# Performance work log

Measured on AMD Instinct MI355X. Metric: run time of the kernel, lower is better.

Reference implementation:

```python
import jax, jax.numpy as jnp
import numpy as np

N_NODES = 100000
N_EDGES = 1600000
IN_F = 128
HEADS1, HID = 8, 8
N_CLASSES = 40


def setup_inputs() -> dict:
    key = jax.random.key(0)
    ks = jax.random.split(key, 12)
    x = jax.random.normal(ks[0], (N_NODES, IN_F), dtype=jnp.float32)
    edge_index = jax.random.randint(ks[1], (2, N_EDGES), 0, N_NODES, dtype=jnp.int32)
    edge_attr = jax.random.uniform(ks[2], (N_EDGES, 1), dtype=jnp.float32)
    s = 0.1
    W1 = jax.random.normal(ks[3], (IN_F, HEADS1 * HID), dtype=jnp.float32) * s
    att_src1 = jax.random.normal(ks[4], (HEADS1, HID), dtype=jnp.float32) * s
    att_dst1 = jax.random.normal(ks[5], (HEADS1, HID), dtype=jnp.float32) * s
    att_edge1 = jax.random.normal(ks[6], (1, HEADS1), dtype=jnp.float32) * s
    W2 = jax.random.normal(ks[7], (HEADS1 * HID, N_CLASSES), dtype=jnp.float32) * s
    att_src2 = jax.random.normal(ks[8], (1, N_CLASSES), dtype=jnp.float32) * s
    att_dst2 = jax.random.normal(ks[9], (1, N_CLASSES), dtype=jnp.float32) * s
    att_edge2 = jax.random.normal(ks[10], (1, 1), dtype=jnp.float32) * s
    return {"x": x, "edge_index": edge_index, "edge_attr": edge_attr,
            "W1": W1, "att_src1": att_src1, "att_dst1": att_dst1, "att_edge1": att_edge1,
            "W2": W2, "att_src2": att_src2, "att_dst2": att_dst2, "att_edge2": att_edge2}


def _egat(x, src, dst, edge_attr, W, a_src, a_dst, a_edge, heads, out_dim, concat):
    """Edge-featured GAT conv: gather -> per-edge attention -> neighborhood softmax -> scatter."""
    n = x.shape[0]
    h = (x @ W).reshape(n, heads, out_dim)                       # [N,H,F]
    h_src = h[src]                                               # [E,H,F]
    logits = (h_src * a_src).sum(-1) + (h[dst] * a_dst).sum(-1)  # [E,H]
    logits = logits + edge_attr @ a_edge                          # edge feature term
    logits = jax.nn.leaky_relu(logits, 0.2)
    m = jax.ops.segment_max(logits, dst, num_segments=n)         # [N,H]
    e = jnp.exp(logits - m[dst])
    denom = jax.ops.segment_sum(e, dst, num_segments=n)
    alpha = e / (denom[dst] + 1e-16)                             # softmax over incoming edges
    out = jax.ops.segment_sum(alpha[:, :, None] * h_src, dst, num_segments=n)  # [N,H,F]
    return out.reshape(n, heads * out_dim) if concat else out.mean(axis=1)


def reference(x, edge_index, edge_attr, W1, att_src1, att_dst1, att_edge1,
              W2, att_src2, att_dst2, att_edge2):
    src, dst = edge_index[0], edge_index[1]
    h = _egat(x, src, dst, edge_attr, W1, att_src1, att_dst1, att_edge1, HEADS1, HID, True)
    h = jax.nn.elu(h)
    out = _egat(h, src, dst, edge_attr, W2, att_src2, att_dst2, att_edge2, 1, N_CLASSES, True)
    return jax.nn.log_softmax(out, axis=1)
```

## Files before the change

### kernel.cpp

```cpp
#include <hip/hip_runtime.h>
#include <math.h>

#define N_NODES 100000
#define N_EDGES 1600000
#define IN_F    128
#define NH1     8
#define HID     8
#define C1      64
#define C2      40

#define EB      2048
#define B1      ((N_EDGES + EB - 1) / EB)
#define NPB     128
#define NBIN    ((N_NODES + NPB - 1) / NPB)
#define S2CAP   2560

#define WPREP_BLKS 44
#define GEMM1_BLKS ((N_NODES / 16 + 3) / 4)

typedef unsigned short ushort_t;
typedef unsigned int uint_t;
typedef _Float16 half_t;
typedef short short8 __attribute__((ext_vector_type(8)));
typedef float f32x4 __attribute__((ext_vector_type(4)));

__device__ __forceinline__ float lrelu(float x) { return x > 0.f ? x : 0.2f * x; }
__device__ __forceinline__ ushort_t f2bf(float f) {
    uint_t u = __float_as_uint(f);
    u = (u + 0x7FFFu + ((u >> 16) & 1u)) >> 16;
    return (ushort_t)u;
}
__device__ __forceinline__ float bf2f(ushort_t s) {
    return __uint_as_float(((uint_t)s) << 16);
}
__device__ __forceinline__ short8 ld8f2bf(const float* p) {
    float4 a = *(const float4*)p;
    float4 b = *(const float4*)(p + 4);
    ushort_t o[8] = {f2bf(a.x), f2bf(a.y), f2bf(a.z), f2bf(a.w),
                     f2bf(b.x), f2bf(b.y), f2bf(b.z), f2bf(b.w)};
    return *(const short8*)o;
}

__global__ __launch_bounds__(256) void k_prep_hist(
    const float* __restrict__ W1, ushort_t* __restrict__ W1p,
    const float* __restrict__ W2, ushort_t* __restrict__ W2p,
    const int* __restrict__ ei, int* __restrict__ Hblk)
{
    int b = blockIdx.x;
    if (b < B1) {
        __shared__ int h[NBIN];
        for (int i = threadIdx.x; i < NBIN; i += 256) h[i] = 0;
        __syncthreads();
        int base = b * EB;
        for (int i = threadIdx.x; i < EB; i += 256) {
            int idx = base + i;
            if (idx < N_EDGES) atomicAdd(&h[((uint_t)ei[N_EDGES + idx]) >> 7], 1);
        }
        __syncthreads();
        for (int i = threadIdx.x; i < NBIN; i += 256)
            Hblk[i * B1 + b] = h[i];
        return;
    }
    int i = (b - B1) * 256 + threadIdx.x;
    if (i < 8192) {
        int j = i & 7, lane = (i >> 3) & 63, nt = (i >> 9) & 3, s = i >> 11;
        int k = s * 32 + (lane >> 4) * 8 + j;
        int n = nt * 16 + (lane & 15);
        W1p[i] = f2bf(W1[k * C1 + n]);
    } else {
        int i2 = i - 8192;
        if (i2 < 3072) {
            int j = i2 & 7, lane = (i2 >> 3) & 63, khalf = (i2 >> 9) & 1, nt = i2 >> 10;
            int n = nt * 16 + (lane & 15);
            int k = khalf * 32 + (lane >> 4) * 8 + j;
            float v = (n < C2) ? W2[k * C2 + n] : 0.f;
            W2p[i2] = f2bf(v);
        }
    }
}

__global__ __launch_bounds__(512) void k_colscan(
    int* __restrict__ Hblk, int* __restrict__ totB)
{
    __shared__ int s[512];
    int bin = blockIdx.x, t = threadIdx.x;
    int run = 0;
    for (int c = 0; c < 2; ++c) {
        int i = c * 512 + t;
        int v = (i < B1) ? Hblk[bin * B1 + i] : 0;
        s[t] = v;
        __syncthreads();
        for (int off = 1; off < 512; off <<= 1) {
            int u = (t >= off) ? s[t - off] : 0;
            __syncthreads();
            s[t] += u;
            __syncthreads();
        }
        if (i < B1) Hblk[bin * B1 + i] = s[t] - v + run;
        int tot = s[511];
        __syncthreads();
        run += tot;
    }
    if (t == 0) totB[bin] = run;
}

__global__ __launch_bounds__(512) void k_basescan(
    const int* __restrict__ totB, int* __restrict__ baseB,
    int* __restrict__ rowptr)
{
    __shared__ int s[512];
    int t = threadIdx.x;
    int run = 0;
    for (int c = 0; c < 2; ++c) {
        int i = c * 512 + t;
        int v = (i < NBIN) ? totB[i] : 0;
        s[t] = v;
        __syncthreads();
        for (int off = 1; off < 512; off <<= 1) {
            int u = (t >= off) ? s[t - off] : 0;
            __syncthreads();
            s[t] += u;
            __syncthreads();
        }
        if (i < NBIN) baseB[i] = s[t] - v + run;
        int tot = s[511];
        __syncthreads();
        run += tot;
    }
    if (t == 0) { baseB[NBIN] = run; rowptr[N_NODES] = run; }
}

__global__ __launch_bounds__(256) void k_gemm1_sc1(
    const float* __restrict__ x, const ushort_t* __restrict__ W1p,
    const float* __restrict__ as1, const float* __restrict__ ad1,
    ushort_t* __restrict__ H1, float* __restrict__ s1, float* __restrict__ d1,
    const int* __restrict__ ei, const float* __restrict__ ea,
    const int* __restrict__ Hblk, const int* __restrict__ baseB,
    int2* __restrict__ coarse)
{
    int b = blockIdx.x;
    int t = threadIdx.x;
    if (b < B1) {
        __shared__ int    cnt[NBIN];
        __shared__ int    loff[NBIN];
        __shared__ int    gof[NBIN];
        __shared__ int    ssc[256];
        __shared__ int2   sbuf[EB];
        __shared__ ushort_t sbin[EB];
        int base = b * EB;
        int nE = min(EB, N_EDGES - base);
        for (int i = t; i < NBIN; i += 256) cnt[i] = 0;
        __syncthreads();
        int myb[EB / 256];
        #pragma unroll
        for (int c = 0; c < EB / 256; ++c) {
            int i = base + c * 256 + t;
            int bn = -1;
            if (i < N_EDGES) {
                bn = ((uint_t)ei[N_EDGES + i]) >> 7;
                atomicAdd(&cnt[bn], 1);
            }
            myb[c] = bn;
        }
        __syncthreads();
        {
            int b4 = t * 4;
            int a0 = (b4 + 0 < NBIN) ? cnt[b4 + 0] : 0;
            int a1 = (b4 + 1 < NBIN) ? cnt[b4 + 1] : 0;
            int a2 = (b4 + 2 < NBIN) ? cnt[b4 + 2] : 0;
            int a3 = (b4 + 3 < NBIN) ? cnt[b4 + 3] : 0;
            int tsum = a0 + a1 + a2 + a3;
            ssc[t] = tsum;
            __syncthreads();
            for (int off = 1; off < 256; off <<= 1) {
                int u = (t >= off) ? ssc[t - off] : 0;
                __syncthreads();
                ssc[t] += u;
                __syncthreads();
            }
            int exc = ssc[t] - tsum;
            if (b4 + 0 < NBIN) loff[b4 + 0] = exc;
            if (b4 + 1 < NBIN) loff[b4 + 1] = exc + a0;
            if (b4 + 2 < NBIN) loff[b4 + 2] = exc + a0 + a1;
            if (b4 + 3 < NBIN) loff[b4 + 3] = exc + a0 + a1 + a2;
        }
        __syncthreads();
        for (int i = t; i < NBIN; i += 256) {
            gof[i] = baseB[i] + Hblk[i * B1 + b] - loff[i];
            cnt[i] = loff[i];
        }
        __syncthreads();
        #pragma unroll
        for (int c = 0; c < EB / 256; ++c) {
            int i = base + c * 256 + t;
            if (i < N_EDGES) {
                int bn = myb[c];
                int s = ei[i];
                int d = ei[N_EDGES + i];
                float e = ea[i];
                int p = atomicAdd(&cnt[bn], 1);
                sbuf[p] = make_int2(s | ((d & (NPB - 1)) << 24), __float_as_int(e));
                sbin[p] = (ushort_t)bn;
            }
        }
        __syncthreads();
        for (int j = t; j < nE; j += 256) {
            int bn = sbin[j];
            coarse[gof[bn] + j] = sbuf[j];
        }
        return;
    }
    int tile = ((b - B1) * 256 + t) >> 6;
    int lane = t & 63;
    if (tile >= N_NODES / 16) return;
    int quad = lane >> 4, lo = lane & 15;
    const float* arow = x + ((size_t)tile * 16 + lo) * IN_F + quad * 8;
    short8 a0 = ld8f2bf(arow);
    short8 a1 = ld8f2bf(arow + 32);
    short8 a2 = ld8f2bf(arow + 64);
    short8 a3 = ld8f2bf(arow + 96);
    f32x4 acc[4] = {{0,0,0,0},{0,0,0,0},{0,0,0,0},{0,0,0,0}};
    #pragma unroll
    for (int nt = 0; nt < 4; ++nt) {
        short8 b0 = *(const short8*)&W1p[((0 * 4 + nt) * 64 + lane) * 8];
        short8 b1 = *(const short8*)&W1p[((1 * 4 + nt) * 64 + lane) * 8];
        short8 b2 = *(const short8*)&W1p[((2 * 4 + nt) * 64 + lane) * 8];
        short8 b3 = *(const short8*)&W1p[((3 * 4 + nt) * 64 + lane) * 8];
        acc[nt] = __builtin_amdgcn_mfma_f32_16x16x32_bf16(a0, b0, acc[nt], 0, 0, 0);
        acc[nt] = __builtin_amdgcn_mfma_f32_16x16x32_bf16(a1, b1, acc[nt], 0, 0, 0);
        acc[nt] = __builtin_amdgcn_mfma_f32_16x16x32_bf16(a2, b2, acc[nt], 0, 0, 0);
        acc[nt] = __builtin_amdgcn_mfma_f32_16x16x32_bf16(a3, b3, acc[nt], 0, 0, 0);
    }
    int nb = tile * 16 + quad * 4;
    float ps[4][4], pd[4][4];
    #pragma unroll
    for (int nt = 0; nt < 4; ++nt) {
        int cb = nt * 16 + lo;
        float av = as1[cb], dv = ad1[cb];
        #pragma unroll
        for (int r = 0; r < 4; ++r) {
            H1[(size_t)(nb + r) * C1 + cb] = f2bf(acc[nt][r]);
            ps[nt][r] = acc[nt][r] * av;
            pd[nt][r] = acc[nt][r] * dv;
        }
    }
    #pragma unroll
    for (int nt = 0; nt < 4; ++nt)
        #pragma unroll
        for (int r = 0; r < 4; ++r)
            #pragma unroll
            for (int off = 1; off < 8; off <<= 1) {
                ps[nt][r] += __shfl_xor(ps[nt][r], off);
                pd[nt][r] += __shfl_xor(pd[nt][r], off);
            }
    if ((lo & 7) == 0) {
        int hh = lo >> 3;
        #pragma unroll
        for (int nt = 0; nt < 4; ++nt) {
            int h = nt * 2 + hh;
            #pragma unroll
            for (int r = 0; r < 4; ++r) {
                s1[(nb + r) * NH1 + h] = ps[nt][r];
                d1[(nb + r) * NH1 + h] = pd[nt][r];
            }
        }
    }
}

__global__ __launch_bounds__(256) void k_scatter2(
    const int2* __restrict__ coarse, const int* __restrict__ baseB,
    int2* __restrict__ edges, int* __restrict__ rowptr)
{
    __shared__ int2 buf[S2CAP];
    __shared__ int h[NPB];
    __shared__ int ofx[NPB];
    __shared__ int ssc[256];
    int bin = blockIdx.x, t = threadIdx.x;
    int s0 = baseB[bin], s1b = baseB[bin + 1];
    int n = s1b - s0;
    if (t < NPB) h[t] = 0;
    __syncthreads();
    for (int j = t; j < n; j += 256)
        atomicAdd(&h[(uint_t)coarse[s0 + j].x >> 24], 1);
    __syncthreads();
    int v = (t < NPB) ? h[t] : 0;
    ssc[t] = v;
    __syncthreads();
    for (int off = 1; off < 256; off <<= 1) {
        int u = (t >= off) ? ssc[t - off] : 0;
        __syncthreads();
        ssc[t] += u;
        __syncthreads();
    }
    int exc = ssc[t] - v;
    if (t < NPB) {
        ofx[t] = exc;
        int node = bin * NPB + t;
        if (node < N_NODES) rowptr[node] = s0 + exc;
        h[t] = exc;
    }
    __syncthreads();
    for (int j = t; j < n; j += 256) {
        int2 c = coarse[s0 + j];
        int ln = (uint_t)c.x >> 24;
        int p = atomicAdd(&h[ln], 1);
        int2 ov = make_int2(c.x & 0x00FFFFFF, c.y);
        if (p < S2CAP) buf[p] = ov;
        else           edges[s0 + p] = ov;
    }
    __syncthreads();
    int nl = n < S2CAP ? n : S2CAP;
    for (int j = t; j < nl; j += 256)
        edges[s0 + j] = buf[j];
}


__global__ __launch_bounds__(256) void k_node1(
    const int* __restrict__ rowptr, const int2* __restrict__ edges,
    const float* __restrict__ s1, const float* __restrict__ d1,
    const float* __restrict__ ae1,
    const ushort_t* __restrict__ H1, ushort_t* __restrict__ out1r)
{
    __shared__ uint_t sm_s[4][64];
    __shared__ float  sm_pf[4][8][65];
    int w = (blockIdx.x * blockDim.x + threadIdx.x) >> 6;
    int lane = threadIdx.x & 63;
    int wv = (threadIdx.x >> 6) & 3;
    if (w >= N_NODES) return;
    int half = lane >> 5, lo32 = lane & 31;
    int h = lo32 >> 2;
    uint_t fb = (uint_t)lo32 << 2;
    int jb = rowptr[w], je = rowptr[w + 1];
    float4 d1a = *(const float4*)(d1 + w * NH1);
    float4 d1b = *(const float4*)(d1 + w * NH1 + 4);
    float4 aea = *(const float4*)(ae1);
    float4 aeb = *(const float4*)(ae1 + 4);
    float den = 0.f, acc0 = 0.f, acc1 = 0.f;
    const float* pfh = sm_pf[wv][h];
    for (int base = jb; base < je; base += 64) {
        int idx = base + lane;
        uint_t soff = 0;
        float pf[8] = {0.f, 0.f, 0.f, 0.f, 0.f, 0.f, 0.f, 0.f};
        if (idx < je) {
            int2 ed = edges[idx];
            soff = (uint_t)ed.x << 7;
            float ea = __int_as_float(ed.y);
            const float* s1r = s1 + (size_t)ed.x * NH1;
            float4 sa = *(const float4*)s1r;
            float4 sb = *(const float4*)(s1r + 4);
            pf[0] = __expf(lrelu(fmaf(ea, aea.x, sa.x + d1a.x)));
            pf[1] = __expf(lrelu(fmaf(ea, aea.y, sa.y + d1a.y)));
            pf[2] = __expf(lrelu(fmaf(ea, aea.z, sa.z + d1a.z)));
            pf[3] = __expf(lrelu(fmaf(ea, aea.w, sa.w + d1a.w)));
            pf[4] = __expf(lrelu(fmaf(ea, aeb.x, sb.x + d1b.x)));
            pf[5] = __expf(lrelu(fmaf(ea, aeb.y, sb.y + d1b.y)));
            pf[6] = __expf(lrelu(fmaf(ea, aeb.z, sb.z + d1b.z)));
            pf[7] = __expf(lrelu(fmaf(ea, aeb.w, sb.w + d1b.w)));
        }
        sm_s[wv][lane] = soff;
        #pragma unroll
        for (int k = 0; k < 8; ++k) sm_pf[wv][k][lane] = pf[k];
        __builtin_amdgcn_wave_barrier();
        int cnt4 = (min(64, je - base) + 3) & ~3;
        for (int e = half; e < cnt4; e += 4) {
            uint_t soA = sm_s[wv][e];
            uint_t soB = sm_s[wv][e + 2];
            float pA = pfh[e];
            float pB = pfh[e + 2];
            uint_t uA = *(const uint_t*)((const char*)H1 + (soA + fb));
            uint_t uB = *(const uint_t*)((const char*)H1 + (soB + fb));
            den += pA + pB;
            acc0 = fmaf(pA, __uint_as_float(uA << 16), acc0);
            acc1 = fmaf(pA, __uint_as_float(uA & 0xffff0000u), acc1);
            acc0 = fmaf(pB, __uint_as_float(uB << 16), acc0);
            acc1 = fmaf(pB, __uint_as_float(uB & 0xffff0000u), acc1);
        }
        __builtin_amdgcn_wave_barrier();
    }
    acc0 += __shfl_xor(acc0, 32);
    acc1 += __shfl_xor(acc1, 32);
    den  += __shfl_xor(den, 32);
    float inv = 1.f / (den + 1e-16f);
    float o0 = acc0 * inv, o1 = acc1 * inv;
    float r0 = o0 > 0.f ? o0 : __expf(o0) - 1.f;
    float r1 = o1 > 0.f ? o1 : __expf(o1) - 1.f;
    if (half == 0) {
        uint_t pk = (uint_t)f2bf(r0) | ((uint_t)f2bf(r1) << 16);
        *(uint_t*)((char*)out1r + (size_t)w * 128 + fb) = pk;
    }
}

__global__ __launch_bounds__(256) void k_gemm2(
    const ushort_t* __restrict__ out1r, const ushort_t* __restrict__ W2p,
    const float* __restrict__ as2, const float* __restrict__ ad2,
    ushort_t* __restrict__ H2, float* __restrict__ s2, float* __restrict__ d2)
{
    int tile = (blockIdx.x * blockDim.x + threadIdx.x) >> 6;
    int lane = threadIdx.x & 63;
    if (tile >= N_NODES / 16) return;
    int quad = lane >> 4, lo = lane & 15;
    const ushort_t* arow = out1r + ((size_t)tile * 16 + lo) * C1 + quad * 8;
    short8 a0 = *(const short8*)arow;
    short8 a1 = *(const short8*)(arow + 32);
    f32x4 acc[3] = {{0,0,0,0},{0,0,0,0},{0,0,0,0}};
    #pragma unroll
    for (int nt = 0; nt < 3; ++nt) {
        short8 b0 = *(const short8*)&W2p[((nt * 2 + 0) * 64 + lane) * 8];
        short8 b1 = *(const short8*)&W2p[((nt * 2 + 1) * 64 + lane) * 8];
        acc[nt] = __builtin_amdgcn_mfma_f32_16x16x32_bf16(a0, b0, acc[nt], 0, 0, 0);
        acc[nt] = __builtin_amdgcn_mfma_f32_16x16x32_bf16(a1, b1, acc[nt], 0, 0, 0);
    }
    float ps0 = 0.f, ps1 = 0.f, ps2 = 0.f, ps3 = 0.f;
    float pd0 = 0.f, pd1 = 0.f, pd2 = 0.f, pd3 = 0.f;
    #pragma unroll
    for (int nt = 0; nt < 3; ++nt) {
        int cb = nt * 16 + lo;
        float a2 = cb < C2 ? as2[cb] : 0.f;
        float b2 = cb < C2 ? ad2[cb] : 0.f;
        float v0 = acc[nt][0], v1 = acc[nt][1], v2 = acc[nt][2], v3 = acc[nt][3];
        int nb = tile * 16 + quad * 4;
        H2[(size_t)(nb + 0) * C1 + cb] = f2bf(v0);
        H2[(size_t)(nb + 1) * C1 + cb] = f2bf(v1);
        H2[(size_t)(nb + 2) * C1 + cb] = f2bf(v2);
        H2[(size_t)(nb + 3) * C1 + cb] = f2bf(v3);
        ps0 = fmaf(v0, a2, ps0); ps1 = fmaf(v1, a2, ps1);
        ps2 = fmaf(v2, a2, ps2); ps3 = fmaf(v3, a2, ps3);
        pd0 = fmaf(v0, b2, pd0); pd1 = fmaf(v1, b2, pd1);
        pd2 = fmaf(v2, b2, pd2); pd3 = fmaf(v3, b2, pd3);
    }
    #pragma unroll
    for (int off = 1; off < 16; off <<= 1) {
        ps0 += __shfl_xor(ps0, off); ps1 += __shfl_xor(ps1, off);
        ps2 += __shfl_xor(ps2, off); ps3 += __shfl_xor(ps3, off);
        pd0 += __shfl_xor(pd0, off); pd1 += __shfl_xor(pd1, off);
        pd2 += __shfl_xor(pd2, off); pd3 += __shfl_xor(pd3, off);
    }
    if (lo == 0) {
        int nb = tile * 16 + quad * 4;
        s2[nb + 0] = ps0; s2[nb + 1] = ps1; s2[nb + 2] = ps2; s2[nb + 3] = ps3;
        d2[nb + 0] = pd0; d2[nb + 1] = pd1; d2[nb + 2] = pd2; d2[nb + 3] = pd3;
    }
}

__global__ __launch_bounds__(256) void k_node2(
    const int* __restrict__ rowptr, const int2* __restrict__ edges,
    const float* __restrict__ s2, const float* __restrict__ d2,
    const float* __restrict__ ae2,
    const ushort_t* __restrict__ H2, float* __restrict__ out)
{
    __shared__ int2 sp[4][64];
    int w = (blockIdx.x * blockDim.x + threadIdx.x) >> 6;
    int lane = threadIdx.x & 63;
    int wv = (threadIdx.x >> 6) & 3;
    if (w >= N_NODES) return;
    int half = lane >> 5, lo32 = lane & 31;
    int fi = lo32 < 20 ? lo32 : 19;
    uint_t fb = (uint_t)fi << 2;
    int jb = rowptr[w], je = rowptr[w + 1];
    float d2v = d2[w];
    float aev = ae2[0];
    float den = 0.f, acc0 = 0.f, acc1 = 0.f;
    for (int base = jb; base < je; base += 64) {
        int idx = base + lane;
        int soff = 0; float p = 0.f;
        if (idx < je) {
            int2 ed = edges[idx];
            soff = ed.x << 7;
            p = __expf(lrelu(s2[ed.x] + d2v + __int_as_float(ed.y) * aev));
        }
        sp[wv][lane] = make_int2(soff, __float_as_int(p));
        __builtin_amdgcn_wave_barrier();
        int cnt4 = (min(64, je - base) + 3) & ~3;
        for (int e = half; e < cnt4; e += 4) {
            int2 edA = sp[wv][e];
            int2 edB = sp[wv][e + 2];
            uint_t uA = *(const uint_t*)((const char*)H2 + ((uint_t)edA.x + fb));
            uint_t uB = *(const uint_t*)((const char*)H2 + ((uint_t)edB.x + fb));
            float pA = __int_as_float(edA.y);
            float pB = __int_as_float(edB.y);
            den += pA + pB;
            acc0 = fmaf(pA, __uint_as_float(uA << 16), acc0);
            acc1 = fmaf(pA, __uint_as_float(uA & 0xffff0000u), acc1);
            acc0 = fmaf(pB, __uint_as_float(uB << 16), acc0);
            acc1 = fmaf(pB, __uint_as_float(uB & 0xffff0000u), acc1);
        }
        __builtin_amdgcn_wave_barrier();
    }
    acc0 += __shfl_xor(acc0, 32);
    acc1 += __shfl_xor(acc1, 32);
    den  += __shfl_xor(den, 32);
    float inv = 1.f / (den + 1e-16f);
    float o0 = acc0 * inv, o1 = acc1 * inv;
    float v0 = lo32 < 20 ? o0 : -INFINITY;
    float v1 = lo32 < 20 ? o1 : -INFINITY;
    float m = fmaxf(v0, v1);
    #pragma unroll
    for (int off = 16; off; off >>= 1) m = fmaxf(m, __shfl_xor(m, off));
    float pp = lo32 < 20 ? __expf(v0 - m) + __expf(v1 - m) : 0.f;
    #pragma unroll
    for (int off = 16; off; off >>= 1) pp += __shfl_xor(pp, off);
    float ls = __logf(pp);
    if (half == 0 && lo32 < 20) {
        float2 st = make_float2(v0 - m - ls, v1 - m - ls);
        *(float2*)(out + (size_t)w * C2 + 2 * fi) = st;
    }
}

extern "C" void kernel_launch(void* const* d_in, const int* in_sizes, int n_in,
                              void* d_out, int out_size, void* d_ws, size_t ws_size,
                              hipStream_t stream)
{
    const float* x   = (const float*)d_in[0];
    const int*   ei  = (const int*)  d_in[1];
    const float* ea  = (const float*)d_in[2];
    const float* W1  = (const float*)d_in[3];
    const float* as1 = (const float*)d_in[4];
    const float* ad1 = (const float*)d_in[5];
    const float* ae1 = (const float*)d_in[6];
    const float* W2  = (const float*)d_in[7];
    const float* as2 = (const float*)d_in[8];
    const float* ad2 = (const float*)d_in[9];
    const float* ae2 = (const float*)d_in[10];
    float* out = (float*)d_out;

    float*    ws     = (float*)d_ws;
    ushort_t* H1     = (ushort_t*)ws;
    ushort_t* H2     = (ushort_t*)ws;
    ushort_t* out1r  = (ushort_t*)(ws + 3200000);
    int*      Hblk   = (int*)(ws + 3200000);
    int*      totB   = (int*)(ws + 3820000);
    int*      baseB  = (int*)(ws + 3821000);
    int2*     coarse = (int2*)(ws + 6400000);
    int2*     edges  = (int2*)(ws + 9600000);
    float*    s1     = ws + 16000000;
    float*    d1     = ws + 16800000;
    int*      rowptr = (int*)(ws + 17600000);
    float*    s2     = ws + 17700008;
    float*    d2     = ws + 17800008;
    ushort_t* W2p    = (ushort_t*)(ws + 17900008);
    ushort_t* W1p    = (ushort_t*)(ws + 17901544);

    k_prep_hist <<<B1 + WPREP_BLKS, 256, 0, stream>>>(
        W1, W1p, W2, W2p, ei, Hblk);
    k_colscan   <<<NBIN, 512, 0, stream>>>(Hblk, totB);
    k_basescan  <<<1, 512, 0, stream>>>(totB, baseB, rowptr);
    k_gemm1_sc1 <<<B1 + GEMM1_BLKS, 256, 0, stream>>>(
        x, W1p, as1, ad1, H1, s1, d1, ei, ea, Hblk, baseB, coarse);
    k_scatter2  <<<NBIN, 256, 0, stream>>>(coarse, baseB, edges, rowptr);
    k_node1     <<<(N_NODES + 3) / 4, 256, 0, stream>>>(rowptr, edges, s1, d1, ae1,
                                                        H1, out1r);
    k_gemm2     <<<(N_NODES / 16 + 3) / 4, 256, 0, stream>>>(out1r, W2p, as2, ad2,
                                                             H2, s2, d2);
    k_node2     <<<(N_NODES + 3) / 4, 256, 0, stream>>>(rowptr, edges, s2, d2, ae2,
                                                        H2, out);
}
```

Before: 286.3 us.

## Process two nodes per wavefront in GAT aggregation kernels and transpose histogram layout

The per-node aggregation kernels now map two destination nodes onto one 64-lane wavefront, each half-wave handling one node's edges in chunks of 32. The cross-half shuffle reduction goes away and the grid is halved. With an average degree of 16, this should waste fewer lanes than one node per wave with 64-edge chunks. The per-block histogram matrix is also transposed to block-major, so the histogram writes and the scatter reads become contiguous while the column scan reads become strided. The risk is divergence when the two paired nodes have very different degrees, since both halves loop to the larger count.

```diff
diff --git a/kernel.cpp b/kernel.cpp
--- a/kernel.cpp
+++ b/kernel.cpp
@@ -17,6 +17,7 @@
 
 #define WPREP_BLKS 44
 #define GEMM1_BLKS ((N_NODES / 16 + 3) / 4)
+#define NPAIR   (N_NODES / 2)
 
 typedef unsigned short ushort_t;
 typedef unsigned int uint_t;
@@ -58,7 +59,7 @@
         }
         __syncthreads();
         for (int i = threadIdx.x; i < NBIN; i += 256)
-            Hblk[i * B1 + b] = h[i];
+            Hblk[b * NBIN + i] = h[i];
         return;
     }
     int i = (b - B1) * 256 + threadIdx.x;
@@ -87,7 +88,7 @@
     int run = 0;
     for (int c = 0; c < 2; ++c) {
         int i = c * 512 + t;
-        int v = (i < B1) ? Hblk[bin * B1 + i] : 0;
+        int v = (i < B1) ? Hblk[i * NBIN + bin] : 0;
         s[t] = v;
         __syncthreads();
         for (int off = 1; off < 512; off <<= 1) {
@@ -96,7 +97,7 @@
             s[t] += u;
             __syncthreads();
         }
-        if (i < B1) Hblk[bin * B1 + i] = s[t] - v + run;
+        if (i < B1) Hblk[i * NBIN + bin] = s[t] - v + run;
         int tot = s[511];
         __syncthreads();
         run += tot;
@@ -186,7 +187,7 @@
         }
         __syncthreads();
         for (int i = t; i < NBIN; i += 256) {
-            gof[i] = baseB[i] + Hblk[i * B1 + b] - loff[i];
+            gof[i] = baseB[i] + Hblk[b * NBIN + i] - loff[i];
             cnt[i] = loff[i];
         }
         __syncthreads();
@@ -273,7 +274,6 @@
 {
     __shared__ int2 buf[S2CAP];
     __shared__ int h[NPB];
-    __shared__ int ofx[NPB];
     __shared__ int ssc[256];
     int bin = blockIdx.x, t = threadIdx.x;
     int s0 = baseB[bin], s1b = baseB[bin + 1];
@@ -294,7 +294,6 @@
     }
     int exc = ssc[t] - v;
     if (t < NPB) {
-        ofx[t] = exc;
         int node = bin * NPB + t;
         if (node < N_NODES) rowptr[node] = s0 + exc;
         h[t] = exc;
@@ -321,28 +320,31 @@
     const float* __restrict__ ae1,
     const ushort_t* __restrict__ H1, ushort_t* __restrict__ out1r)
 {
-    __shared__ uint_t sm_s[4][64];
-    __shared__ float  sm_pf[4][8][65];
-    int w = (blockIdx.x * blockDim.x + threadIdx.x) >> 6;
+    __shared__ uint_t sm_s[4][2][33];
+    __shared__ float  sm_pf[4][2][8][33];
+    int w2 = (blockIdx.x * blockDim.x + threadIdx.x) >> 6;
     int lane = threadIdx.x & 63;
     int wv = (threadIdx.x >> 6) & 3;
-    if (w >= N_NODES) return;
+    if (w2 >= NPAIR) return;
     int half = lane >> 5, lo32 = lane & 31;
+    int node = 2 * w2 + half;
     int h = lo32 >> 2;
     uint_t fb = (uint_t)lo32 << 2;
-    int jb = rowptr[w], je = rowptr[w + 1];
-    float4 d1a = *(const float4*)(d1 + w * NH1);
-    float4 d1b = *(const float4*)(d1 + w * NH1 + 4);
+    int jb = rowptr[node], je = rowptr[node + 1];
+    int cnt = je - jb;
+    int maxc = max(cnt, __shfl_xor(cnt, 32));
+    float4 d1a = *(const float4*)(d1 + node * NH1);
+    float4 d1b = *(const float4*)(d1 + node * NH1 + 4);
     float4 aea = *(const float4*)(ae1);
     float4 aeb = *(const float4*)(ae1 + 4);
     float den = 0.f, acc0 = 0.f, acc1 = 0.f;
-    const float* pfh = sm_pf[wv][h];
-    for (int base = jb; base < je; base += 64) {
-        int idx = base + lane;
+    const float* pfh = &sm_pf[wv][half][h][0];
+    for (int base = 0; base < maxc; base += 32) {
+        int loc = base + lo32;
         uint_t soff = 0;
         float pf[8] = {0.f, 0.f, 0.f, 0.f, 0.f, 0.f, 0.f, 0.f};
-        if (idx < je) {
-            int2 ed = edges[idx];
+        if (loc < cnt) {
+            int2 ed = edges[jb + loc];
             soff = (uint_t)ed.x << 7;
             float ea = __int_as_float(ed.y);
             const float* s1r = s1 + (size_t)ed.x * NH1;
@@ -357,16 +359,16 @@
             pf[6] = __expf(lrelu(fmaf(ea, aeb.z, sb.z + d1b.z)));
             pf[7] = __expf(lrelu(fmaf(ea, aeb.w, sb.w + d1b.w)));
         }
-        sm_s[wv][lane] = soff;
+        sm_s[wv][half][lo32] = soff;
         #pragma unroll
-        for (int k = 0; k < 8; ++k) sm_pf[wv][k][lane] = pf[k];
+        for (int k = 0; k < 8; ++k) sm_pf[wv][half][k][lo32] = pf[k];
         __builtin_amdgcn_wave_barrier();
-        int cnt4 = (min(64, je - base) + 3) & ~3;
-        for (int e = half; e < cnt4; e += 4) {
-            uint_t soA = sm_s[wv][e];
-            uint_t soB = sm_s[wv][e + 2];
+        int steps = (min(32, maxc - base) + 1) & ~1;
+        for (int e = 0; e < steps; e += 2) {
+            uint_t soA = sm_s[wv][half][e];
+            uint_t soB = sm_s[wv][half][e + 1];
             float pA = pfh[e];
-            float pB = pfh[e + 2];
+            float pB = pfh[e + 1];
             uint_t uA = *(const uint_t*)((const char*)H1 + (soA + fb));
             uint_t uB = *(const uint_t*)((const char*)H1 + (soB + fb));
             den += pA + pB;
@@ -377,17 +379,12 @@
         }
         __builtin_amdgcn_wave_barrier();
     }
-    acc0 += __shfl_xor(acc0, 32);
-    acc1 += __shfl_xor(acc1, 32);
-    den  += __shfl_xor(den, 32);
     float inv = 1.f / (den + 1e-16f);
     float o0 = acc0 * inv, o1 = acc1 * inv;
     float r0 = o0 > 0.f ? o0 : __expf(o0) - 1.f;
     float r1 = o1 > 0.f ? o1 : __expf(o1) - 1.f;
-    if (half == 0) {
-        uint_t pk = (uint_t)f2bf(r0) | ((uint_t)f2bf(r1) << 16);
-        *(uint_t*)((char*)out1r + (size_t)w * 128 + fb) = pk;
-    }
+    uint_t pk = (uint_t)f2bf(r0) | ((uint_t)f2bf(r1) << 16);
+    *(uint_t*)((char*)out1r + (size_t)node * 128 + fb) = pk;
 }
 
 __global__ __launch_bounds__(256) void k_gemm2(
@@ -448,32 +445,35 @@
     const float* __restrict__ ae2,
     const ushort_t* __restrict__ H2, float* __restrict__ out)
 {
-    __shared__ int2 sp[4][64];
-    int w = (blockIdx.x * blockDim.x + threadIdx.x) >> 6;
+    __shared__ int2 sp[4][2][33];
+    int w2 = (blockIdx.x * blockDim.x + threadIdx.x) >> 6;
     int lane = threadIdx.x & 63;
     int wv = (threadIdx.x >> 6) & 3;
-    if (w >= N_NODES) return;
+    if (w2 >= NPAIR) return;
     int half = lane >> 5, lo32 = lane & 31;
+    int node = 2 * w2 + half;
     int fi = lo32 < 20 ? lo32 : 19;
     uint_t fb = (uint_t)fi << 2;
-    int jb = rowptr[w], je = rowptr[w + 1];
-    float d2v = d2[w];
+    int jb = rowptr[node], je = rowptr[node + 1];
+    int cnt = je - jb;
+    int maxc = max(cnt, __shfl_xor(cnt, 32));
+    float d2v = d2[node];
     float aev = ae2[0];
     float den = 0.f, acc0 = 0.f, acc1 = 0.f;
-    for (int base = jb; base < je; base += 64) {
-        int idx = base + lane;
+    for (int base = 0; base < maxc; base += 32) {
+        int loc = base + lo32;
         int soff = 0; float p = 0.f;
-        if (idx < je) {
-            int2 ed = edges[idx];
+        if (loc < cnt) {
+            int2 ed = edges[jb + loc];
             soff = ed.x << 7;
             p = __expf(lrelu(s2[ed.x] + d2v + __int_as_float(ed.y) * aev));
         }
-        sp[wv][lane] = make_int2(soff, __float_as_int(p));
+        sp[wv][half][lo32] = make_int2(soff, __float_as_int(p));
         __builtin_amdgcn_wave_barrier();
-        int cnt4 = (min(64, je - base) + 3) & ~3;
-        for (int e = half; e < cnt4; e += 4) {
-            int2 edA = sp[wv][e];
-            int2 edB = sp[wv][e + 2];
+        int steps = (min(32, maxc - base) + 1) & ~1;
+        for (int e = 0; e < steps; e += 2) {
+            int2 edA = sp[wv][half][e];
+            int2 edB = sp[wv][half][e + 1];
             uint_t uA = *(const uint_t*)((const char*)H2 + ((uint_t)edA.x + fb));
             uint_t uB = *(const uint_t*)((const char*)H2 + ((uint_t)edB.x + fb));
             float pA = __int_as_float(edA.y);
@@ -486,9 +486,6 @@
         }
         __builtin_amdgcn_wave_barrier();
     }
-    acc0 += __shfl_xor(acc0, 32);
-    acc1 += __shfl_xor(acc1, 32);
-    den  += __shfl_xor(den, 32);
     float inv = 1.f / (den + 1e-16f);
     float o0 = acc0 * inv, o1 = acc1 * inv;
     float v0 = lo32 < 20 ? o0 : -INFINITY;
@@ -500,9 +497,9 @@
     #pragma unroll
     for (int off = 16; off; off >>= 1) pp += __shfl_xor(pp, off);
     float ls = __logf(pp);
-    if (half == 0 && lo32 < 20) {
+    if (lo32 < 20) {
         float2 st = make_float2(v0 - m - ls, v1 - m - ls);
-        *(float2*)(out + (size_t)w * C2 + 2 * fi) = st;
+        *(float2*)(out + (size_t)node * C2 + 2 * fi) = st;
     }
 }
 
@@ -547,10 +544,10 @@
     k_gemm1_sc1 <<<B1 + GEMM1_BLKS, 256, 0, stream>>>(
         x, W1p, as1, ad1, H1, s1, d1, ei, ea, Hblk, baseB, coarse);
     k_scatter2  <<<NBIN, 256, 0, stream>>>(coarse, baseB, edges, rowptr);
-    k_node1     <<<(N_NODES + 3) / 4, 256, 0, stream>>>(rowptr, edges, s1, d1, ae1,
-                                                        H1, out1r);
+    k_node1     <<<(NPAIR + 3) / 4, 256, 0, stream>>>(rowptr, edges, s1, d1, ae1,
+                                                      H1, out1r);
     k_gemm2     <<<(N_NODES / 16 + 3) / 4, 256, 0, stream>>>(out1r, W2p, as2, ad2,
                                                              H2, s2, d2);
-    k_node2     <<<(N_NODES + 3) / 4, 256, 0, stream>>>(rowptr, edges, s2, d2, ae2,
-                                                        H2, out);
-}
+    k_node2     <<<(NPAIR + 3) / 4, 256, 0, stream>>>(rowptr, edges, s2, d2, ae2,
+                                                      H2, out);
+}
```

Result: faster. 272.9 us (-4.7%).
